# Kernel optimization log

Measured on AMD Instinct MI355X. Metric: run time of the kernel, lower is better.

The kernel has to match this reference:

```python
import jax, jax.numpy as jnp
import numpy as np

N, ID, OD, M, S, L = 65536, 16, 8, 1024, 8, 64


def setup_inputs() -> dict:
    key = jax.random.key(0)
    k1, k2, k3, k4, k5, k6 = jax.random.split(key, 6)
    return {
        "x": jax.random.normal(k1, (N, ID), dtype=jnp.float32),
        "inducing_locations": jax.random.uniform(k2, (M, ID), dtype=jnp.float32),
        "inducing_weights": jax.random.normal(k3, (S, OD, M), dtype=jnp.float32),
        "prior_frequency": jax.random.normal(k4, (OD, ID, L), dtype=jnp.float32),
        "prior_phase": jax.random.uniform(k5, (OD, L), dtype=jnp.float32, maxval=2 * np.pi),
        "prior_weights": jax.random.normal(k6, (S, OD, L), dtype=jnp.float32),
    }


def _rbf_matrix(x, z):
    # ExponentiatedQuadratic with amplitude=1, length_scale=1:
    # k(x,z) = exp(-0.5 * ||x - z||^2)
    x2 = jnp.sum(x * x, axis=-1)[:, None]          # [N,1]
    z2 = jnp.sum(z * z, axis=-1)[None, :]          # [1,M]
    sq = jnp.maximum(x2 + z2 - 2.0 * (x @ z.T), 0.0)
    return jnp.exp(-0.5 * sq)                      # [N,M]


def reference(x, inducing_locations, inducing_weights, prior_frequency, prior_phase, prior_weights):
    # ---- prior (random Fourier features) ----
    # spectral_weights for unit RBF: outer_weights = ones((OD,L)), inner_weights = ones((ID,))
    # rescaled_x = x / 1 = x
    # basis_fn_inner_prod: [OD, N, L]
    inner = jnp.einsum('ni,oil->onl', x, prior_frequency)
    basis_fn = jnp.cos(inner + prior_phase[:, None, :])              # [OD,N,L]
    basis_weight = jnp.sqrt(2.0 / prior_frequency.shape[-1]) * prior_weights  # [S,OD,L]
    f_prior = jnp.einsum('onl,sol->son', basis_fn, basis_weight)     # [S,OD,N]

    # ---- data term (kernel matrix + matvec) ----
    K = _rbf_matrix(x, inducing_locations)                           # [N,M]
    f_data = jnp.einsum('nm,som->son', K, inducing_weights)          # [S,OD,N]

    return f_prior + f_data
```

## Files before the change

### kernel.cpp

```cpp
#include <hip/hip_runtime.h>
#include <hip/hip_bf16.h>

#define N_PTS 65536

typedef __attribute__((ext_vector_type(8))) short short8;
typedef __attribute__((ext_vector_type(4))) short short4v;
typedef __attribute__((ext_vector_type(4))) float float4v;

__device__ __forceinline__ short f2b(float f) {
    __hip_bfloat16 h = __float2bfloat16(f);
    return *(short*)&h;
}
__device__ __forceinline__ float b2f(short s) {
    __hip_bfloat16 h = *(__hip_bfloat16*)&s;
    return __bfloat162float(h);
}

__global__ __launch_bounds__(256) void prep_kernel(
    const float* __restrict__ z, const float* __restrict__ W,
    const float* __restrict__ F, const float* __restrict__ pw,
    short* __restrict__ zb, short* __restrict__ FbB,
    short* __restrict__ BWd, short* __restrict__ Wtb,
    float* __restrict__ z2)
{
    int t = blockIdx.x * 256 + threadIdx.x;
    if (t < 1024) {
        float s = 0.f;
        #pragma unroll
        for (int i = 0; i < 16; i++) {
            short b = f2b(z[t * 16 + i]);
            zb[t * 16 + i] = b;
            float v = b2f(b);
            s += v * v;
        }
        z2[t] = s;
    } else if (t < 9216) {
        int p = t - 1024;
        int o = p >> 10, l = (p >> 4) & 63, i = p & 15;
        FbB[p] = f2b(F[o * 1024 + i * 64 + l]);
    } else if (t < 41984) {
        int p = t - 9216;
        int so = p >> 9, ol = p & 511, o = ol >> 6, l = ol & 63;
        float v = ((so & 7) == o) ? 0.17677669529663687f * pw[so * 64 + l] : 0.f;
        BWd[p] = f2b(v);
    } else if (t < 107520) {
        int p = t - 41984;
        Wtb[p] = f2b(W[p]);
    }
}

__global__ __launch_bounds__(256, 4) void fused_kernel(
    const float* __restrict__ x, const float* __restrict__ ph,
    const short* __restrict__ zb, const short* __restrict__ FbB,
    const short* __restrict__ BWd, const short* __restrict__ Wtb,
    const float* __restrict__ z2, float* __restrict__ out)
{
    __shared__ __align__(16) short tileL[64 * 68];
    __shared__ float x2c[64];

    const int tid = threadIdx.x;
    const int lane = tid & 63, w = tid >> 6;
    const int q = lane >> 4, c = lane & 15;
    const int n0 = blockIdx.x * 64;

    if (tid < 64) {
        float s = 0.f;
        const float4v* xr = (const float4v*)(x + (size_t)(n0 + tid) * 16);
        #pragma unroll
        for (int k = 0; k < 4; k++) {
            float4v v = xr[k];
            float a0 = b2f(f2b(v.x)), a1 = b2f(f2b(v.y));
            float a2 = b2f(f2b(v.z)), a3 = b2f(f2b(v.w));
            s += a0 * a0 + a1 * a1 + a2 * a2 + a3 * a3;
        }
        x2c[tid] = s;
    }

    short8 ax = (short8)0;
    if (q < 2) {
        const float4v* xp = (const float4v*)(x + (size_t)(n0 + 16 * w + c) * 16 + q * 8);
        float4v v0 = xp[0], v1 = xp[1];
        ax[0] = f2b(v0.x); ax[1] = f2b(v0.y); ax[2] = f2b(v0.z); ax[3] = f2b(v0.w);
        ax[4] = f2b(v1.x); ax[5] = f2b(v1.y); ax[6] = f2b(v1.z); ax[7] = f2b(v1.w);
    }

    float4v acc[4];
    #pragma unroll
    for (int i = 0; i < 4; i++) acc[i] = (float4v)(0.f);

    __syncthreads();

    float x2r[4];
    #pragma unroll
    for (int r = 0; r < 4; r++) x2r[r] = x2c[16 * w + q * 4 + r];

    for (int o = 0; o < 8; o++) {
        #pragma unroll
        for (int lt = 0; lt < 4; lt++) {
            short8 bf = (short8)0;
            if (q < 2) bf = *(const short8*)(FbB + ((o * 64 + lt * 16 + c) * 16 + q * 8));
            float4v d = __builtin_amdgcn_mfma_f32_16x16x32_bf16(ax, bf, (float4v)(0.f), 0, 0, 0);
            float phv = ph[o * 64 + lt * 16 + c];
            #pragma unroll
            for (int r = 0; r < 4; r++) {
                float cv = __cosf(d[r] + phv);
                tileL[(16 * w + q * 4 + r) * 68 + lt * 16 + c] = f2b(cv);
            }
        }
        __syncthreads();
        #pragma unroll
        for (int ks = 0; ks < 2; ks++) {
            short8 aw = *(const short8*)(BWd + ((16 * w + c) * 512 + o * 64 + ks * 32 + q * 8));
            #pragma unroll
            for (int nt = 0; nt < 4; nt++) {
                const short* tp = tileL + (nt * 16 + c) * 68 + ks * 32 + q * 8;
                short4v lo = *(const short4v*)tp;
                short4v hi = *(const short4v*)(tp + 4);
                short8 bb;
                bb[0] = lo[0]; bb[1] = lo[1]; bb[2] = lo[2]; bb[3] = lo[3];
                bb[4] = hi[0]; bb[5] = hi[1]; bb[6] = hi[2]; bb[7] = hi[3];
                acc[nt] = __builtin_amdgcn_mfma_f32_16x16x32_bf16(aw, bb, acc[nt], 0, 0, 0);
            }
        }
        __syncthreads();
    }

    for (int mc = 0; mc < 16; mc++) {
        int m0 = mc * 64;
        #pragma unroll
        for (int mt = 0; mt < 4; mt++) {
            short8 bz = (short8)0;
            if (q < 2) bz = *(const short8*)(zb + ((m0 + mt * 16 + c) * 16 + q * 8));
            float4v d = __builtin_amdgcn_mfma_f32_16x16x32_bf16(ax, bz, (float4v)(0.f), 0, 0, 0);
            float z2v = z2[m0 + mt * 16 + c];
            #pragma unroll
            for (int r = 0; r < 4; r++) {
                float dist = fmaxf(x2r[r] + z2v - 2.f * d[r], 0.f);
                float e = __expf(-0.5f * dist);
                tileL[(16 * w + q * 4 + r) * 68 + mt * 16 + c] = f2b(e);
            }
        }
        __syncthreads();
        #pragma unroll
        for (int ks = 0; ks < 2; ks++) {
            short8 aw = *(const short8*)(Wtb + ((16 * w + c) * 1024 + m0 + ks * 32 + q * 8));
            #pragma unroll
            for (int nt = 0; nt < 4; nt++) {
                const short* tp = tileL + (nt * 16 + c) * 68 + ks * 32 + q * 8;
                short4v lo = *(const short4v*)tp;
                short4v hi = *(const short4v*)(tp + 4);
                short8 bb;
                bb[0] = lo[0]; bb[1] = lo[1]; bb[2] = lo[2]; bb[3] = lo[3];
                bb[4] = hi[0]; bb[5] = hi[1]; bb[6] = hi[2]; bb[7] = hi[3];
                acc[nt] = __builtin_amdgcn_mfma_f32_16x16x32_bf16(aw, bb, acc[nt], 0, 0, 0);
            }
        }
        __syncthreads();
    }

    #pragma unroll
    for (int nt = 0; nt < 4; nt++) {
        #pragma unroll
        for (int r = 0; r < 4; r++) {
            out[(size_t)(16 * w + q * 4 + r) * N_PTS + n0 + nt * 16 + c] = acc[nt][r];
        }
    }
}

extern "C" void kernel_launch(void* const* d_in, const int* in_sizes, int n_in,
                              void* d_out, int out_size, void* d_ws, size_t ws_size,
                              hipStream_t stream) {
    const float* x  = (const float*)d_in[0];
    const float* z  = (const float*)d_in[1];
    const float* W  = (const float*)d_in[2];
    const float* F  = (const float*)d_in[3];
    const float* ph = (const float*)d_in[4];
    const float* pw = (const float*)d_in[5];
    float* out = (float*)d_out;

    char* ws = (char*)d_ws;
    short* zb  = (short*)(ws);
    short* FbB = (short*)(ws + 32768);
    short* BWd = (short*)(ws + 49152);
    short* Wtb = (short*)(ws + 114688);
    float* z2  = (float*)(ws + 245760);

    prep_kernel<<<420, 256, 0, stream>>>(z, W, F, pw, zb, FbB, BWd, Wtb, z2);
    fused_kernel<<<1024, 256, 0, stream>>>(x, ph, zb, FbB, BWd, Wtb, z2, out);
}
```

Measured before the change: 131.3 us.

## Fold bias terms into MFMA accumulator, double-buffer LDS tiles, widen chunks

The phase offset and the scaled squared-norm terms now go into the MFMA accumulator's initial value, so the elementwise work before cos/exp is removed. The data term uses exp2 with z pre-scaled by log2(e). The fmax clamp on the distance is dropped, so a slightly negative distance can give a kernel value a little above one. The LDS tile is double-buffered and chunks grow from 64 to 128 columns, which cuts the barriers to one per chunk. Phases are cached in LDS, and tile reads become single 16-byte loads; the cost is more LDS per block and more registers.

```diff
diff --git a/kernel.cpp b/kernel.cpp
--- a/kernel.cpp
+++ b/kernel.cpp
@@ -2,10 +2,16 @@
 #include <hip/hip_bf16.h>
 
 #define N_PTS 65536
+#define LOG2E 1.4426950408889634f
 
 typedef __attribute__((ext_vector_type(8))) short short8;
-typedef __attribute__((ext_vector_type(4))) short short4v;
 typedef __attribute__((ext_vector_type(4))) float float4v;
+
+#if __has_builtin(__builtin_amdgcn_exp2f)
+#define EXP2F(x) __builtin_amdgcn_exp2f(x)
+#else
+#define EXP2F(x) exp2f(x)
+#endif
 
 __device__ __forceinline__ short f2b(float f) {
     __hip_bfloat16 h = __float2bfloat16(f);
@@ -21,30 +27,34 @@
     const float* __restrict__ F, const float* __restrict__ pw,
     short* __restrict__ zb, short* __restrict__ FbB,
     short* __restrict__ BWd, short* __restrict__ Wtb,
-    float* __restrict__ z2)
+    float* __restrict__ z2h)
 {
     int t = blockIdx.x * 256 + threadIdx.x;
-    if (t < 1024) {
+    if (t < 16384) {
+        zb[t] = f2b(LOG2E * z[t]);
+    } else if (t < 17408) {
+        int m = t - 16384;
+        const float4v* zp = (const float4v*)(z + (size_t)m * 16);
         float s = 0.f;
         #pragma unroll
-        for (int i = 0; i < 16; i++) {
-            short b = f2b(z[t * 16 + i]);
-            zb[t * 16 + i] = b;
-            float v = b2f(b);
-            s += v * v;
+        for (int k = 0; k < 4; k++) {
+            float4v v = zp[k];
+            float a0 = b2f(f2b(v.x)), a1 = b2f(f2b(v.y));
+            float a2 = b2f(f2b(v.z)), a3 = b2f(f2b(v.w));
+            s += a0 * a0 + a1 * a1 + a2 * a2 + a3 * a3;
         }
-        z2[t] = s;
-    } else if (t < 9216) {
-        int p = t - 1024;
+        z2h[m] = 0.5f * LOG2E * s;
+    } else if (t < 25600) {
+        int p = t - 17408;
         int o = p >> 10, l = (p >> 4) & 63, i = p & 15;
         FbB[p] = f2b(F[o * 1024 + i * 64 + l]);
-    } else if (t < 41984) {
-        int p = t - 9216;
-        int so = p >> 9, ol = p & 511, o = ol >> 6, l = ol & 63;
-        float v = ((so & 7) == o) ? 0.17677669529663687f * pw[so * 64 + l] : 0.f;
+    } else if (t < 58368) {
+        int p = t - 25600;
+        int so = p >> 9, ol = p & 511, o = ol >> 6;
+        float v = ((so & 7) == o) ? 0.17677669529663687f * pw[so * 64 + (ol & 63)] : 0.f;
         BWd[p] = f2b(v);
-    } else if (t < 107520) {
-        int p = t - 41984;
+    } else if (t < 123904) {
+        int p = t - 58368;
         Wtb[p] = f2b(W[p]);
     }
 }
@@ -53,9 +63,10 @@
     const float* __restrict__ x, const float* __restrict__ ph,
     const short* __restrict__ zb, const short* __restrict__ FbB,
     const short* __restrict__ BWd, const short* __restrict__ Wtb,
-    const float* __restrict__ z2, float* __restrict__ out)
+    const float* __restrict__ z2h, float* __restrict__ out)
 {
-    __shared__ __align__(16) short tileL[64 * 68];
+    __shared__ __align__(16) short tile[2][64 * 136];
+    __shared__ float phc[512];
     __shared__ float x2c[64];
 
     const int tid = threadIdx.x;
@@ -63,6 +74,7 @@
     const int q = lane >> 4, c = lane & 15;
     const int n0 = blockIdx.x * 64;
 
+    for (int i = tid; i < 512; i += 256) phc[i] = ph[i];
     if (tid < 64) {
         float s = 0.f;
         const float4v* xr = (const float4v*)(x + (size_t)(n0 + tid) * 16);
@@ -73,7 +85,7 @@
             float a2 = b2f(f2b(v.z)), a3 = b2f(f2b(v.w));
             s += a0 * a0 + a1 * a1 + a2 * a2 + a3 * a3;
         }
-        x2c[tid] = s;
+        x2c[tid] = 0.5f * LOG2E * s;
     }
 
     short8 ax = (short8)0;
@@ -90,72 +102,69 @@
 
     __syncthreads();
 
-    float x2r[4];
     #pragma unroll
-    for (int r = 0; r < 4; r++) x2r[r] = x2c[16 * w + q * 4 + r];
-
-    for (int o = 0; o < 8; o++) {
+    for (int p = 0; p < 4; p++) {
+        short* tl = tile[p & 1];
         #pragma unroll
-        for (int lt = 0; lt < 4; lt++) {
+        for (int lt = 0; lt < 8; lt++) {
             short8 bf = (short8)0;
-            if (q < 2) bf = *(const short8*)(FbB + ((o * 64 + lt * 16 + c) * 16 + q * 8));
-            float4v d = __builtin_amdgcn_mfma_f32_16x16x32_bf16(ax, bf, (float4v)(0.f), 0, 0, 0);
-            float phv = ph[o * 64 + lt * 16 + c];
+            if (q < 2) bf = *(const short8*)(FbB + ((p * 128 + lt * 16 + c) * 16 + q * 8));
+            float phv = phc[p * 128 + lt * 16 + c];
+            float4v c0 = {phv, phv, phv, phv};
+            float4v d = __builtin_amdgcn_mfma_f32_16x16x32_bf16(ax, bf, c0, 0, 0, 0);
             #pragma unroll
-            for (int r = 0; r < 4; r++) {
-                float cv = __cosf(d[r] + phv);
-                tileL[(16 * w + q * 4 + r) * 68 + lt * 16 + c] = f2b(cv);
+            for (int r = 0; r < 4; r++)
+                tl[(16 * w + q * 4 + r) * 136 + lt * 16 + c] = f2b(__cosf(d[r]));
+        }
+        short8 aw[4];
+        #pragma unroll
+        for (int ks = 0; ks < 4; ks++)
+            aw[ks] = *(const short8*)(BWd + ((16 * w + c) * 512 + p * 128 + ks * 32 + q * 8));
+        __syncthreads();
+        #pragma unroll
+        for (int ks = 0; ks < 4; ks++) {
+            #pragma unroll
+            for (int nt = 0; nt < 4; nt++) {
+                short8 bb = *(const short8*)(tl + (nt * 16 + c) * 136 + ks * 32 + q * 8);
+                acc[nt] = __builtin_amdgcn_mfma_f32_16x16x32_bf16(aw[ks], bb, acc[nt], 0, 0, 0);
             }
         }
+    }
+
+    float mx2[4];
+    #pragma unroll
+    for (int r = 0; r < 4; r++) mx2[r] = -x2c[16 * w + q * 4 + r];
+
+    #pragma unroll
+    for (int mc = 0; mc < 8; mc++) {
+        short* tl = tile[mc & 1];
+        int m0 = mc * 128;
+        #pragma unroll
+        for (int mt = 0; mt < 8; mt++) {
+            short8 bz = (short8)0;
+            if (q < 2) bz = *(const short8*)(zb + ((m0 + mt * 16 + c) * 16 + q * 8));
+            float z2v = z2h[m0 + mt * 16 + c];
+            float4v c0;
+            #pragma unroll
+            for (int r = 0; r < 4; r++) c0[r] = mx2[r] - z2v;
+            float4v d = __builtin_amdgcn_mfma_f32_16x16x32_bf16(ax, bz, c0, 0, 0, 0);
+            #pragma unroll
+            for (int r = 0; r < 4; r++)
+                tl[(16 * w + q * 4 + r) * 136 + mt * 16 + c] = f2b(EXP2F(d[r]));
+        }
+        short8 aw[4];
+        #pragma unroll
+        for (int ks = 0; ks < 4; ks++)
+            aw[ks] = *(const short8*)(Wtb + ((16 * w + c) * 1024 + m0 + ks * 32 + q * 8));
         __syncthreads();
         #pragma unroll
-        for (int ks = 0; ks < 2; ks++) {
-            short8 aw = *(const short8*)(BWd + ((16 * w + c) * 512 + o * 64 + ks * 32 + q * 8));
+        for (int ks = 0; ks < 4; ks++) {
             #pragma unroll
             for (int nt = 0; nt < 4; nt++) {
-                const short* tp = tileL + (nt * 16 + c) * 68 + ks * 32 + q * 8;
-                short4v lo = *(const short4v*)tp;
-                short4v hi = *(const short4v*)(tp + 4);
-                short8 bb;
-                bb[0] = lo[0]; bb[1] = lo[1]; bb[2] = lo[2]; bb[3] = lo[3];
-                bb[4] = hi[0]; bb[5] = hi[1]; bb[6] = hi[2]; bb[7] = hi[3];
-                acc[nt] = __builtin_amdgcn_mfma_f32_16x16x32_bf16(aw, bb, acc[nt], 0, 0, 0);
+                short8 bb = *(const short8*)(tl + (nt * 16 + c) * 136 + ks * 32 + q * 8);
+                acc[nt] = __builtin_amdgcn_mfma_f32_16x16x32_bf16(aw[ks], bb, acc[nt], 0, 0, 0);
             }
         }
-        __syncthreads();
-    }
-
-    for (int mc = 0; mc < 16; mc++) {
-        int m0 = mc * 64;
-        #pragma unroll
-        for (int mt = 0; mt < 4; mt++) {
-            short8 bz = (short8)0;
-            if (q < 2) bz = *(const short8*)(zb + ((m0 + mt * 16 + c) * 16 + q * 8));
-            float4v d = __builtin_amdgcn_mfma_f32_16x16x32_bf16(ax, bz, (float4v)(0.f), 0, 0, 0);
-            float z2v = z2[m0 + mt * 16 + c];
-            #pragma unroll
-            for (int r = 0; r < 4; r++) {
-                float dist = fmaxf(x2r[r] + z2v - 2.f * d[r], 0.f);
-                float e = __expf(-0.5f * dist);
-                tileL[(16 * w + q * 4 + r) * 68 + mt * 16 + c] = f2b(e);
-            }
-        }
-        __syncthreads();
-        #pragma unroll
-        for (int ks = 0; ks < 2; ks++) {
-            short8 aw = *(const short8*)(Wtb + ((16 * w + c) * 1024 + m0 + ks * 32 + q * 8));
-            #pragma unroll
-            for (int nt = 0; nt < 4; nt++) {
-                const short* tp = tileL + (nt * 16 + c) * 68 + ks * 32 + q * 8;
-                short4v lo = *(const short4v*)tp;
-                short4v hi = *(const short4v*)(tp + 4);
-                short8 bb;
-                bb[0] = lo[0]; bb[1] = lo[1]; bb[2] = lo[2]; bb[3] = lo[3];
-                bb[4] = hi[0]; bb[5] = hi[1]; bb[6] = hi[2]; bb[7] = hi[3];
-                acc[nt] = __builtin_amdgcn_mfma_f32_16x16x32_bf16(aw, bb, acc[nt], 0, 0, 0);
-            }
-        }
-        __syncthreads();
     }
 
     #pragma unroll
@@ -183,8 +192,8 @@
     short* FbB = (short*)(ws + 32768);
     short* BWd = (short*)(ws + 49152);
     short* Wtb = (short*)(ws + 114688);
-    float* z2  = (float*)(ws + 245760);
+    float* z2h = (float*)(ws + 245760);
 
-    prep_kernel<<<420, 256, 0, stream>>>(z, W, F, pw, zb, FbB, BWd, Wtb, z2);
-    fused_kernel<<<1024, 256, 0, stream>>>(x, ph, zb, FbB, BWd, Wtb, z2, out);
+    prep_kernel<<<484, 256, 0, stream>>>(z, W, F, pw, zb, FbB, BWd, Wtb, z2h);
+    fused_kernel<<<1024, 256, 0, stream>>>(x, ph, zb, FbB, BWd, Wtb, z2h, out);
 }
```

New measurement: 122.8 us. 6.5% less time.
